# Optimization experiments

Hardware: AMD Instinct MI355X
Metric: run time of the kernel (lower is better)

The kernel has to match this reference:

```python
import jax, jax.numpy as jnp
import numpy as np

EOS = 1e-10
N_NODES = 100000
N_EDGES = 1600000
IN_DIM = 256
HID = 64
ALPHA = 0.1
TEMP = 1.0
BIAS = 1e-4


def setup_inputs() -> dict:
    key = jax.random.key(0)
    k1, k2, k3, k4, k5 = jax.random.split(key, 5)
    features = jax.random.normal(k1, (N_NODES, IN_DIM), dtype=jnp.float32)
    edges = jax.random.randint(k2, (2, N_EDGES), 0, N_NODES, dtype=jnp.int64)
    noise = jax.random.uniform(k3, (N_EDGES,), dtype=jnp.float32)
    # params: embedding Linear(input_dim, hidden) and edge_mlp Linear(2*hidden, 1)
    W_emb = jax.random.normal(k4, (IN_DIM, HID), dtype=jnp.float32) / np.sqrt(IN_DIM)
    b_emb = jnp.zeros((HID,), dtype=jnp.float32)
    W_edge = jax.random.normal(k5, (2 * HID,), dtype=jnp.float32) / np.sqrt(2 * HID)
    b_edge = jnp.zeros((), dtype=jnp.float32)
    return {"features": features, "edges": edges, "noise": noise,
            "W_emb": W_emb, "b_emb": b_emb, "W_edge": W_edge, "b_edge": b_edge}


def _edge_weight_norm_both(src, dst, w, n_nodes):
    # DGL EdgeWeightNorm(norm='both'): w_e / sqrt(outdeg_w(src) * indeg_w(dst))
    deg_out = jax.ops.segment_sum(w, src, num_segments=n_nodes)
    deg_in = jax.ops.segment_sum(w, dst, num_segments=n_nodes)
    return w / jnp.sqrt(deg_out[src] * deg_in[dst])


def reference(features, edges, noise, W_emb, b_emb, W_edge, b_edge):
    src, dst = edges[0], edges[1]
    E = src.shape[0]
    # node embedding: relu(Linear(features))
    h = jax.nn.relu(features @ W_emb + b_emb)  # [N, H]
    # edge score: edge_mlp(cat(h[u], h[v])) symmetrized.
    # split W_edge -> score = h[u]@W1 + h[v]@W2 + b  (avoids materializing concat)
    p1 = h @ W_edge[:HID]   # [N]
    p2 = h @ W_edge[HID:]   # [N]
    s1 = p1[src] + p2[dst] + b_edge
    s2 = p1[dst] + p2[src] + b_edge
    raw = (s1 + s2) * 0.5   # [E]
    # gumbel sigmoid sampling
    eps = (BIAS - (1.0 - BIAS)) * noise + (1.0 - BIAS)
    gate = jnp.log(eps) - jnp.log1p(-eps)
    weights_lp = jax.nn.sigmoid((gate + raw) / TEMP)  # [E]
    weights_hp = 1.0 - weights_lp
    # weight_to_adj: add self loops with weight 1, then EdgeWeightNorm 'both'
    loop = jnp.arange(N_NODES, dtype=src.dtype)
    src_f = jnp.concatenate([src, loop])
    dst_f = jnp.concatenate([dst, loop])
    ones_n = jnp.ones((N_NODES,), dtype=weights_lp.dtype)
    w_lp_full = jnp.concatenate([weights_lp, ones_n]) + EOS
    w_lp_norm = _edge_weight_norm_both(src_f, dst_f, w_lp_full, N_NODES)
    w_hp_full = jnp.concatenate([weights_hp, ones_n]) + EOS
    w_hp_norm = _edge_weight_norm_both(src_f, dst_f, w_hp_full, N_NODES)
    w_hp_norm = w_hp_norm * (-ALPHA)
    w_hp_norm = w_hp_norm.at[E:].set(1.0)  # self-loop weights forced to 1
    return (w_lp_norm, w_hp_norm, weights_lp, weights_hp)
```

## Files before the change

kernel.cpp:

```cpp
#include <hip/hip_runtime.h>
#include <hip/hip_bf16.h>
#include <math.h>

#define N_NODESC 100000
#define N_EDGESC 1600000
#define IN_DIMC 256
#define HIDC 64
#define ALPHAC 0.1f
#define BIASC 1e-4f
#define EOSC 1e-10f

#define MC (N_EDGESC + N_NODESC)
#define NBUCK 400
#define BSHIFT 8
#define BMASK 255
#define BCAP 5120u
#define W20SCALE 1048576.0f
#define W20INV (1.0f / 1048576.0f)
#define SUMMASK ((1ull << 40) - 1)
#define CNTONE (1ull << 40)
#define EPB 8

typedef __attribute__((ext_vector_type(8))) short short8;
typedef __attribute__((ext_vector_type(4))) float f32x4;

#define WT_STRIDE 264

__device__ inline void load_edge(const int* __restrict__ edges, int e, int is64,
                                 int& src, int& dst) {
    if (is64) {
        const int2 a = ((const int2*)edges)[e];
        const int2 b = ((const int2*)edges)[N_EDGESC + e];
        src = a.x; dst = b.x;
    } else {
        src = edges[e];
        dst = edges[N_EDGESC + e];
    }
}

__device__ inline short pkbf(float x) {
    union { __hip_bfloat16 b; short s; } u;
    u.b = __float2bfloat16(x);
    return u.s;
}

__global__ __launch_bounds__(256, 3) void node_kernel(
    const float* __restrict__ features,
    const float* __restrict__ W_emb,
    const float* __restrict__ b_emb,
    const float* __restrict__ W_edge,
    const int* __restrict__ edges,
    float* __restrict__ q,
    unsigned* __restrict__ cursor,
    int* __restrict__ flag) {
    __shared__ __align__(16) short Wt[HIDC * WT_STRIDE];
    const int tid = threadIdx.x;
    if (blockIdx.x == 0) {
        if (tid == 0) {
            int z = 0;
            #pragma unroll
            for (int i = 0; i < 16; ++i) z |= edges[2 * i + 1];
            *flag = (z == 0) ? 1 : 0;
        }
        for (int b = tid; b < 2 * NBUCK; b += 256) cursor[b] = 0u;
    }
    {
        const float4* Wg = (const float4*)W_emb;
        #pragma unroll
        for (int i = 0; i < 16; ++i) {
            const int f4 = tid + 256 * i;
            const float4 g = Wg[f4];
            const int flat = 4 * f4;
            const int k = flat >> 6;
            const int j0 = flat & 63;
            Wt[(j0 + 0) * WT_STRIDE + k] = pkbf(g.x);
            Wt[(j0 + 1) * WT_STRIDE + k] = pkbf(g.y);
            Wt[(j0 + 2) * WT_STRIDE + k] = pkbf(g.z);
            Wt[(j0 + 3) * WT_STRIDE + k] = pkbf(g.w);
        }
    }
    const int lane = tid & 63;
    const int wave = tid >> 6;
    const int quad = lane >> 4;
    const int m = lane & 15;
    f32x4 accA[4], accB[4];
    float wsum4[4];
    #pragma unroll
    for (int nt = 0; nt < 4; ++nt) {
        const int j = m + 16 * nt;
        const float b = b_emb[j];
        accA[nt] = (f32x4){b, b, b, b};
        accB[nt] = (f32x4){b, b, b, b};
        wsum4[nt] = W_edge[j] + W_edge[HIDC + j];
    }
    __syncthreads();

    const int node0A = blockIdx.x * 128 + wave * 16;
    const int node0B = node0A + 64;
    const float* frA = features + (size_t)min(node0A + m, N_NODESC - 1) * IN_DIMC;
    const float* frB = features + (size_t)min(node0B + m, N_NODESC - 1) * IN_DIMC;

    #pragma unroll
    for (int ks = 0; ks < 8; ++ks) {
        const int kk = ks * 32 + quad * 8;
        const float4 fa0 = *(const float4*)(frA + kk);
        const float4 fb0 = *(const float4*)(frA + kk + 4);
        const float4 fa1 = *(const float4*)(frB + kk);
        const float4 fb1 = *(const float4*)(frB + kk + 4);
        short8 afA, afB;
        afA[0] = pkbf(fa0.x); afA[1] = pkbf(fa0.y);
        afA[2] = pkbf(fa0.z); afA[3] = pkbf(fa0.w);
        afA[4] = pkbf(fb0.x); afA[5] = pkbf(fb0.y);
        afA[6] = pkbf(fb0.z); afA[7] = pkbf(fb0.w);
        afB[0] = pkbf(fa1.x); afB[1] = pkbf(fa1.y);
        afB[2] = pkbf(fa1.z); afB[3] = pkbf(fa1.w);
        afB[4] = pkbf(fb1.x); afB[5] = pkbf(fb1.y);
        afB[6] = pkbf(fb1.z); afB[7] = pkbf(fb1.w);
        #pragma unroll
        for (int nt = 0; nt < 4; ++nt) {
            const short8 bf =
                *(const short8*)&Wt[(m + 16 * nt) * WT_STRIDE + kk];
            accA[nt] = __builtin_amdgcn_mfma_f32_16x16x32_bf16(afA, bf, accA[nt],
                                                               0, 0, 0);
            accB[nt] = __builtin_amdgcn_mfma_f32_16x16x32_bf16(afB, bf, accB[nt],
                                                               0, 0, 0);
        }
    }

    #pragma unroll
    for (int r = 0; r < 4; ++r) {
        float sA = 0.f, sB = 0.f;
        #pragma unroll
        for (int nt = 0; nt < 4; ++nt) {
            sA = fmaf(fmaxf(accA[nt][r], 0.f), wsum4[nt], sA);
            sB = fmaf(fmaxf(accB[nt][r], 0.f), wsum4[nt], sB);
        }
        sA += __shfl_xor(sA, 1); sA += __shfl_xor(sA, 2);
        sA += __shfl_xor(sA, 4); sA += __shfl_xor(sA, 8);
        sB += __shfl_xor(sB, 1); sB += __shfl_xor(sB, 2);
        sB += __shfl_xor(sB, 4); sB += __shfl_xor(sB, 8);
        if (m == 0) {
            const int nA = node0A + quad * 4 + r;
            const int nB = node0B + quad * 4 + r;
            if (nA < N_NODESC) q[nA] = sA;
            if (nB < N_NODESC) q[nB] = sB;
        }
    }
}

__global__ __launch_bounds__(256) void edge_scatter(
    const int* __restrict__ edges,
    const float* __restrict__ noise,
    const float* __restrict__ b_edge,
    const float* __restrict__ q,
    unsigned* __restrict__ cursor,
    unsigned* __restrict__ recS,
    unsigned* __restrict__ recD,
    float* __restrict__ out,
    const int* __restrict__ flag) {
    __shared__ unsigned hist[2][4][NBUCK];
    __shared__ unsigned wbase[2][4][NBUCK];
    const int tid = threadIdx.x;
    const int wave = tid >> 6;
    for (int i = tid; i < 2 * 4 * NBUCK; i += 256)
        ((unsigned*)hist)[i] = 0u;
    __syncthreads();
    const int is64 = *flag;
    const float be = b_edge[0];
    const int e0 = blockIdx.x * (256 * EPB) + tid;

    int sA[EPB], dA[EPB];
    #pragma unroll
    for (int i = 0; i < EPB; ++i) {
        const int e = e0 + i * 256;
        sA[i] = -1;
        if (e < N_EDGESC) load_edge(edges, e, is64, sA[i], dA[i]);
    }
    float qs[EPB], qd[EPB];
    #pragma unroll
    for (int i = 0; i < EPB; ++i) {
        if (sA[i] >= 0) { qs[i] = q[sA[i]]; qd[i] = q[dA[i]]; }
    }
    float wlpA[EPB];
    unsigned rkS[EPB], rkD[EPB];
    #pragma unroll
    for (int i = 0; i < EPB; ++i) {
        if (sA[i] >= 0) {
            const int e = e0 + i * 256;
            const float raw = 0.5f * (qs[i] + qd[i]) + be;
            const float u = noise[e];
            const float eps = (BIASC - (1.0f - BIASC)) * u + (1.0f - BIASC);
            const float gate = logf(eps) - log1pf(-eps);
            const float wlp = 1.0f / (1.0f + expf(-(gate + raw)));
            wlpA[i] = wlp;
            out[2 * MC + e] = wlp;
            out[2 * MC + N_EDGESC + e] = 1.0f - wlp;
            rkS[i] = atomicAdd(&hist[0][wave][sA[i] >> BSHIFT], 1u);
            rkD[i] = atomicAdd(&hist[1][wave][dA[i] >> BSHIFT], 1u);
        }
    }
    __syncthreads();
    for (int b = tid; b < NBUCK; b += 256) {
        const unsigned h0 = hist[0][0][b], h1 = hist[0][1][b];
        const unsigned h2 = hist[0][2][b], h3 = hist[0][3][b];
        const unsigned base = atomicAdd(&cursor[b], h0 + h1 + h2 + h3);
        wbase[0][0][b] = base;
        wbase[0][1][b] = base + h0;
        wbase[0][2][b] = base + h0 + h1;
        wbase[0][3][b] = base + h0 + h1 + h2;
    }
    for (int b = tid; b < NBUCK; b += 256) {
        const unsigned h0 = hist[1][0][b], h1 = hist[1][1][b];
        const unsigned h2 = hist[1][2][b], h3 = hist[1][3][b];
        const unsigned base = atomicAdd(&cursor[NBUCK + b], h0 + h1 + h2 + h3);
        wbase[1][0][b] = base;
        wbase[1][1][b] = base + h0;
        wbase[1][2][b] = base + h0 + h1;
        wbase[1][3][b] = base + h0 + h1 + h2;
    }
    __syncthreads();
    #pragma unroll
    for (int i = 0; i < EPB; ++i) {
        if (sA[i] >= 0) {
            const int s = sA[i], d = dA[i];
            const unsigned w20 =
                min((unsigned)(wlpA[i] * W20SCALE + 0.5f), 0xFFFFFu);
            const unsigned pS = wbase[0][wave][s >> BSHIFT] + rkS[i];
            const unsigned pD = wbase[1][wave][d >> BSHIFT] + rkD[i];
            if (pS < BCAP)
                recS[(unsigned)(s >> BSHIFT) * BCAP + pS] =
                    ((unsigned)(s & BMASK) << 20) | w20;
            if (pD < BCAP)
                recD[(unsigned)(d >> BSHIFT) * BCAP + pD] =
                    ((unsigned)(d & BMASK) << 20) | w20;
        }
    }
}

__global__ __launch_bounds__(256) void gather_kernel(
    const unsigned* __restrict__ recS,
    const unsigned* __restrict__ recD,
    const unsigned* __restrict__ cursor,
    float2* __restrict__ rS,
    float2* __restrict__ rD) {
    __shared__ unsigned long long table[256];
    const int bid = blockIdx.x;
    const int isD = bid >= NBUCK;
    const int bkt = isD ? bid - NBUCK : bid;
    const unsigned* rec = (isD ? recD : recS) + (unsigned)bkt * BCAP;
    const unsigned cnt = min(cursor[isD ? NBUCK + bkt : bkt], BCAP);
    const int tid = threadIdx.x;
    table[tid] = 0ull;
    __syncthreads();
    for (unsigned i = tid; i < cnt; i += 256) {
        const unsigned r = rec[i];
        atomicAdd(&table[r >> 20], CNTONE | (unsigned long long)(r & 0xFFFFFu));
    }
    __syncthreads();
    float2* dstp = isD ? rD : rS;
    const int node = (bkt << BSHIFT) + tid;
    if (node < N_NODESC) {
        const unsigned long long a = table[tid];
        const float sum = (float)(a & SUMMASK) * W20INV;
        const float cf = (float)(a >> 40);
        float2 r;
        r.x = rsqrtf(1.0f + sum);
        r.y = rsqrtf(1.0f + cf - sum);
        dstp[node] = r;
    }
}

__global__ __launch_bounds__(256) void final_kernel(
    const int* __restrict__ edges,
    const float2* __restrict__ rS,
    const float2* __restrict__ rD,
    float* __restrict__ out,
    const int* __restrict__ flag) {
    const int tid = threadIdx.x;
    const int i0 = blockIdx.x * 1024 + tid;
    const int is64 = *flag;
    int sA[4], dA[4];
    float wl[4], wh[4];
    #pragma unroll
    for (int j = 0; j < 4; ++j) {
        const int i = i0 + j * 256;
        sA[j] = -1;
        if (i < N_EDGESC) {
            load_edge(edges, i, is64, sA[j], dA[j]);
        } else if (i < MC) {
            sA[j] = dA[j] = i - N_EDGESC;
        }
    }
    #pragma unroll
    for (int j = 0; j < 4; ++j) {
        const int i = i0 + j * 256;
        if (i < N_EDGESC) {
            wl[j] = out[2 * MC + i] + EOSC;
            wh[j] = out[2 * MC + N_EDGESC + i] + EOSC;
        } else {
            wl[j] = 1.0f + EOSC;
        }
    }
    float2 a[4], b[4];
    #pragma unroll
    for (int j = 0; j < 4; ++j) {
        if (sA[j] >= 0) { a[j] = rS[sA[j]]; b[j] = rD[dA[j]]; }
    }
    #pragma unroll
    for (int j = 0; j < 4; ++j) {
        const int i = i0 + j * 256;
        if (sA[j] >= 0) {
            out[i] = wl[j] * a[j].x * b[j].x;
            out[MC + i] = (i < N_EDGESC)
                              ? -ALPHAC * wh[j] * a[j].y * b[j].y
                              : 1.0f;
        }
    }
}

extern "C" void kernel_launch(void* const* d_in, const int* in_sizes, int n_in,
                              void* d_out, int out_size, void* d_ws, size_t ws_size,
                              hipStream_t stream) {
    const float* features = (const float*)d_in[0];
    const int* edges      = (const int*)d_in[1];
    const float* noise    = (const float*)d_in[2];
    const float* W_emb    = (const float*)d_in[3];
    const float* b_emb    = (const float*)d_in[4];
    const float* W_edge   = (const float*)d_in[5];
    const float* b_edge   = (const float*)d_in[6];
    float* out = (float*)d_out;
    char* ws = (char*)d_ws;

    float* q = (float*)ws;
    float2* rS = (float2*)(ws + 400000);
    float2* rD = (float2*)(ws + 1200000);
    int* flag = (int*)(ws + 2000000);
    unsigned* cursor = (unsigned*)(ws + 2000064);
    unsigned* recS = (unsigned*)(ws + 2097152);
    unsigned* recD = (unsigned*)(ws + 10289152);

    node_kernel<<<782, 256, 0, stream>>>(features, W_emb, b_emb, W_edge, edges,
                                         q, cursor, flag);
    edge_scatter<<<(N_EDGESC + 256 * EPB - 1) / (256 * EPB), 256, 0, stream>>>(
        edges, noise, b_edge, q, cursor, recS, recD, out, flag);
    gather_kernel<<<2 * NBUCK, 256, 0, stream>>>(recS, recD, cursor, rS, rD);
    final_kernel<<<(MC + 1023) / 1024, 256, 0, stream>>>(edges, rS, rD, out, flag);
}
```

Before: 260.6 us.

## Pack src/dst bucket cursors into one 64-bit atomic and fuse self-loop outputs into gather

Merges the separate src and dst bucket cursors into a single 64-bit counter, so each scatter block issues one global atomic per bucket instead of two. The gather kernel now handles both the src and dst tables of a bucket in one block, and only the used buckets get a block. The same kernel writes the self-loop output entries directly. The final kernel then covers only real edges and derives the high-pass weight as 1 minus the low-pass weight instead of reading it back, which removes one global load per edge. The gather kernel now runs fewer, larger blocks, which may lower parallelism in that stage.

```diff
diff --git a/kernel.cpp b/kernel.cpp
--- a/kernel.cpp
+++ b/kernel.cpp
@@ -12,6 +12,7 @@
 
 #define MC (N_EDGESC + N_NODESC)
 #define NBUCK 400
+#define NBUCK_USED 391
 #define BSHIFT 8
 #define BMASK 255
 #define BCAP 5120u
@@ -51,7 +52,7 @@
     const float* __restrict__ W_edge,
     const int* __restrict__ edges,
     float* __restrict__ q,
-    unsigned* __restrict__ cursor,
+    unsigned long long* __restrict__ cursor64,
     int* __restrict__ flag) {
     __shared__ __align__(16) short Wt[HIDC * WT_STRIDE];
     const int tid = threadIdx.x;
@@ -62,7 +63,7 @@
             for (int i = 0; i < 16; ++i) z |= edges[2 * i + 1];
             *flag = (z == 0) ? 1 : 0;
         }
-        for (int b = tid; b < 2 * NBUCK; b += 256) cursor[b] = 0u;
+        for (int b = tid; b < NBUCK; b += 256) cursor64[b] = 0ull;
     }
     {
         const float4* Wg = (const float4*)W_emb;
@@ -153,7 +154,7 @@
     const float* __restrict__ noise,
     const float* __restrict__ b_edge,
     const float* __restrict__ q,
-    unsigned* __restrict__ cursor,
+    unsigned long long* __restrict__ cursor64,
     unsigned* __restrict__ recS,
     unsigned* __restrict__ recD,
     float* __restrict__ out,
@@ -201,22 +202,24 @@
     }
     __syncthreads();
     for (int b = tid; b < NBUCK; b += 256) {
-        const unsigned h0 = hist[0][0][b], h1 = hist[0][1][b];
-        const unsigned h2 = hist[0][2][b], h3 = hist[0][3][b];
-        const unsigned base = atomicAdd(&cursor[b], h0 + h1 + h2 + h3);
-        wbase[0][0][b] = base;
-        wbase[0][1][b] = base + h0;
-        wbase[0][2][b] = base + h0 + h1;
-        wbase[0][3][b] = base + h0 + h1 + h2;
-    }
-    for (int b = tid; b < NBUCK; b += 256) {
-        const unsigned h0 = hist[1][0][b], h1 = hist[1][1][b];
-        const unsigned h2 = hist[1][2][b], h3 = hist[1][3][b];
-        const unsigned base = atomicAdd(&cursor[NBUCK + b], h0 + h1 + h2 + h3);
-        wbase[1][0][b] = base;
-        wbase[1][1][b] = base + h0;
-        wbase[1][2][b] = base + h0 + h1;
-        wbase[1][3][b] = base + h0 + h1 + h2;
+        const unsigned s0 = hist[0][0][b], s1 = hist[0][1][b];
+        const unsigned s2 = hist[0][2][b], s3 = hist[0][3][b];
+        const unsigned d0 = hist[1][0][b], d1 = hist[1][1][b];
+        const unsigned d2 = hist[1][2][b], d3 = hist[1][3][b];
+        const unsigned long long add =
+            (unsigned long long)(s0 + s1 + s2 + s3) |
+            ((unsigned long long)(d0 + d1 + d2 + d3) << 32);
+        const unsigned long long old = atomicAdd(&cursor64[b], add);
+        const unsigned baseS = (unsigned)old;
+        const unsigned baseD = (unsigned)(old >> 32);
+        wbase[0][0][b] = baseS;
+        wbase[0][1][b] = baseS + s0;
+        wbase[0][2][b] = baseS + s0 + s1;
+        wbase[0][3][b] = baseS + s0 + s1 + s2;
+        wbase[1][0][b] = baseD;
+        wbase[1][1][b] = baseD + d0;
+        wbase[1][2][b] = baseD + d0 + d1;
+        wbase[1][3][b] = baseD + d0 + d1 + d2;
     }
     __syncthreads();
     #pragma unroll
@@ -240,33 +243,48 @@
 __global__ __launch_bounds__(256) void gather_kernel(
     const unsigned* __restrict__ recS,
     const unsigned* __restrict__ recD,
-    const unsigned* __restrict__ cursor,
+    const unsigned long long* __restrict__ cursor64,
     float2* __restrict__ rS,
-    float2* __restrict__ rD) {
-    __shared__ unsigned long long table[256];
-    const int bid = blockIdx.x;
-    const int isD = bid >= NBUCK;
-    const int bkt = isD ? bid - NBUCK : bid;
-    const unsigned* rec = (isD ? recD : recS) + (unsigned)bkt * BCAP;
-    const unsigned cnt = min(cursor[isD ? NBUCK + bkt : bkt], BCAP);
+    float2* __restrict__ rD,
+    float* __restrict__ out) {
+    __shared__ unsigned long long table[512];
+    const int bkt = blockIdx.x;
+    const unsigned long long c = cursor64[bkt];
+    const unsigned cntS = min((unsigned)c, BCAP);
+    const unsigned cntD = min((unsigned)(c >> 32), BCAP);
+    const unsigned* rs = recS + (unsigned)bkt * BCAP;
+    const unsigned* rd = recD + (unsigned)bkt * BCAP;
     const int tid = threadIdx.x;
     table[tid] = 0ull;
-    __syncthreads();
-    for (unsigned i = tid; i < cnt; i += 256) {
-        const unsigned r = rec[i];
+    table[tid + 256] = 0ull;
+    __syncthreads();
+    for (unsigned i = tid; i < cntS; i += 256) {
+        const unsigned r = rs[i];
         atomicAdd(&table[r >> 20], CNTONE | (unsigned long long)(r & 0xFFFFFu));
     }
-    __syncthreads();
-    float2* dstp = isD ? rD : rS;
+    for (unsigned i = tid; i < cntD; i += 256) {
+        const unsigned r = rd[i];
+        atomicAdd(&table[256 + (r >> 20)],
+                  CNTONE | (unsigned long long)(r & 0xFFFFFu));
+    }
+    __syncthreads();
     const int node = (bkt << BSHIFT) + tid;
     if (node < N_NODESC) {
-        const unsigned long long a = table[tid];
-        const float sum = (float)(a & SUMMASK) * W20INV;
-        const float cf = (float)(a >> 40);
-        float2 r;
-        r.x = rsqrtf(1.0f + sum);
-        r.y = rsqrtf(1.0f + cf - sum);
-        dstp[node] = r;
+        const unsigned long long aS = table[tid];
+        const unsigned long long aD = table[tid + 256];
+        const float sumS = (float)(aS & SUMMASK) * W20INV;
+        const float cS = (float)(aS >> 40);
+        const float sumD = (float)(aD & SUMMASK) * W20INV;
+        const float cD = (float)(aD >> 40);
+        float2 vS, vD;
+        vS.x = rsqrtf(1.0f + sumS);
+        vS.y = rsqrtf(1.0f + cS - sumS);
+        vD.x = rsqrtf(1.0f + sumD);
+        vD.y = rsqrtf(1.0f + cD - sumD);
+        rS[node] = vS;
+        rD[node] = vD;
+        out[N_EDGESC + node] = (1.0f + EOSC) * vS.x * vD.x;
+        out[MC + N_EDGESC + node] = 1.0f;
     }
 }
 
@@ -285,20 +303,15 @@
     for (int j = 0; j < 4; ++j) {
         const int i = i0 + j * 256;
         sA[j] = -1;
-        if (i < N_EDGESC) {
-            load_edge(edges, i, is64, sA[j], dA[j]);
-        } else if (i < MC) {
-            sA[j] = dA[j] = i - N_EDGESC;
-        }
+        if (i < N_EDGESC) load_edge(edges, i, is64, sA[j], dA[j]);
     }
     #pragma unroll
     for (int j = 0; j < 4; ++j) {
         const int i = i0 + j * 256;
-        if (i < N_EDGESC) {
-            wl[j] = out[2 * MC + i] + EOSC;
-            wh[j] = out[2 * MC + N_EDGESC + i] + EOSC;
-        } else {
-            wl[j] = 1.0f + EOSC;
+        if (sA[j] >= 0) {
+            const float wlp = out[2 * MC + i];
+            wl[j] = wlp + EOSC;
+            wh[j] = (1.0f - wlp) + EOSC;
         }
     }
     float2 a[4], b[4];
@@ -311,9 +324,7 @@
         const int i = i0 + j * 256;
         if (sA[j] >= 0) {
             out[i] = wl[j] * a[j].x * b[j].x;
-            out[MC + i] = (i < N_EDGESC)
-                              ? -ALPHAC * wh[j] * a[j].y * b[j].y
-                              : 1.0f;
+            out[MC + i] = -ALPHAC * wh[j] * a[j].y * b[j].y;
         }
     }
 }
@@ -335,14 +346,16 @@
     float2* rS = (float2*)(ws + 400000);
     float2* rD = (float2*)(ws + 1200000);
     int* flag = (int*)(ws + 2000000);
-    unsigned* cursor = (unsigned*)(ws + 2000064);
+    unsigned long long* cursor64 = (unsigned long long*)(ws + 2000064);
     unsigned* recS = (unsigned*)(ws + 2097152);
     unsigned* recD = (unsigned*)(ws + 10289152);
 
     node_kernel<<<782, 256, 0, stream>>>(features, W_emb, b_emb, W_edge, edges,
-                                         q, cursor, flag);
+                                         q, cursor64, flag);
     edge_scatter<<<(N_EDGESC + 256 * EPB - 1) / (256 * EPB), 256, 0, stream>>>(
-        edges, noise, b_edge, q, cursor, recS, recD, out, flag);
-    gather_kernel<<<2 * NBUCK, 256, 0, stream>>>(recS, recD, cursor, rS, rD);
-    final_kernel<<<(MC + 1023) / 1024, 256, 0, stream>>>(edges, rS, rD, out, flag);
-}
+        edges, noise, b_edge, q, cursor64, recS, recD, out, flag);
+    gather_kernel<<<NBUCK_USED, 256, 0, stream>>>(recS, recD, cursor64, rS, rD,
+                                                  out);
+    final_kernel<<<(N_EDGESC + 1023) / 1024, 256, 0, stream>>>(edges, rS, rD,
+                                                               out, flag);
+}
```

After: 264.4 us. No clear change (+1.5%).
